# Optimization experiments

Hardware: AMD Instinct MI355X
Metric: run time of the kernel (lower is better)

The kernel has to match this reference:

```python
import jax, jax.numpy as jnp
import numpy as np
import math

B, S, D = 4, 1024, 1024
H, DH = 16, 64
DFF = 4 * D
NEG = -1e9


def _layernorm(x, g, b, eps=1e-5):
    mu = jnp.mean(x, axis=-1, keepdims=True)
    var = jnp.var(x, axis=-1, keepdims=True)
    return (x - mu) * jax.lax.rsqrt(var + eps) * g + b


def setup_inputs() -> dict:
    key = jax.random.key(0)
    ks = jax.random.split(key, 12)
    inp = {
        "input": jax.random.normal(ks[0], (B, S, D), dtype=jnp.float32),
        # additive causal mask: 0 on/below diagonal, -1e9 above
        "causal_mask": jnp.where(
            jnp.tril(jnp.ones((S, S), dtype=bool)), 0.0, NEG
        ).astype(jnp.float32)[None, None],
        # additive padding mask: last 64 tokens of each sequence are padding
        "padding_mask": jnp.where(jnp.arange(S) < S - 64, 0.0, NEG)
        .astype(jnp.float32)[None, None, None, :]
        .repeat(B, axis=0),
        "ln1_g": jnp.ones((D,), jnp.float32), "ln1_b": jnp.zeros((D,), jnp.float32),
        "ln2_g": jnp.ones((D,), jnp.float32), "ln2_b": jnp.zeros((D,), jnp.float32),
        "ln3_g": jnp.ones((D,), jnp.float32), "ln3_b": jnp.zeros((D,), jnp.float32),
        "Wq": jax.random.normal(ks[1], (D, H * DH), jnp.float32) * 0.02,
        "bq": jnp.zeros((H * DH,), jnp.float32),
        "Wk": jax.random.normal(ks[2], (D, H * DH), jnp.float32) * 0.02,
        "bk": jnp.zeros((H * DH,), jnp.float32),
        "Wv": jax.random.normal(ks[3], (D, H * DH), jnp.float32) * 0.02,
        "bv": jnp.zeros((H * DH,), jnp.float32),
        "Wo": jax.random.normal(ks[4], (H * DH, D), jnp.float32) * 0.02,
        "bo": jnp.zeros((D,), jnp.float32),
        "W1": jax.random.normal(ks[5], (D, DFF), jnp.float32) * 0.02,
        "b1": jnp.zeros((DFF,), jnp.float32),
        "W2": jax.random.normal(ks[6], (DFF, D), jnp.float32) * 0.02,
        "b2": jnp.zeros((D,), jnp.float32),
    }
    return inp


def reference(input, causal_mask, padding_mask,
              ln1_g, ln1_b, ln2_g, ln2_b, ln3_g, ln3_b,
              Wq, bq, Wk, bk, Wv, bv, Wo, bo, W1, b1, W2, b2):
    x = _layernorm(input, ln1_g, ln1_b)
    b, s, _ = x.shape

    def heads(y):  # [b,s,H*DH] -> [b,H,s,DH]
        return y.reshape(b, s, H, DH).transpose(0, 2, 1, 3)

    q = heads(x @ Wq + bq)
    k = heads(x @ Wk + bk)
    v = heads(x @ Wv + bv)

    logits = jnp.einsum('bhqd,bhkd->bhqk', q, k) / math.sqrt(DH)
    logits = logits + causal_mask + padding_mask
    probs = jax.nn.softmax(logits, axis=-1)
    attn = jnp.einsum('bhqk,bhkd->bhqd', probs, v)
    attn = attn.transpose(0, 2, 1, 3).reshape(b, s, H * DH)  # b s (h d)
    attn_out = attn @ Wo + bo

    x = x + _layernorm(attn_out, ln2_g, ln2_b)
    h = _layernorm(x, ln3_g, ln3_b)
    x = x + (jax.nn.gelu(h @ W1 + b1, approximate=False) @ W2 + b2)
    return x
```

## Files before the change

kernel.cpp:

```cpp
#include <hip/hip_runtime.h>
#include <hip/hip_bf16.h>

typedef __hip_bfloat16 bf16;
typedef __bf16 bf16x8 __attribute__((ext_vector_type(8)));
typedef float f32x4 __attribute__((ext_vector_type(4)));

#define DEV __device__ __forceinline__

DEV int swz(int r, int k) { return r * 64 + (k ^ ((r & 7) << 3)); }

#define GLOAD_LDS16(gaddr, laddr)                                              \
  __builtin_amdgcn_global_load_lds(                                            \
      (const __attribute__((address_space(1))) void*)(gaddr),                  \
      (__attribute__((address_space(3))) void*)(laddr), 16, 0, 0)

__global__ void prep_kernel(
    const float* __restrict__ Wq, const float* __restrict__ Wk,
    const float* __restrict__ Wv, const float* __restrict__ Wo,
    const float* __restrict__ bq, const float* __restrict__ bk,
    const float* __restrict__ bv,
    bf16* __restrict__ WqkvT, bf16* __restrict__ WoT, float* __restrict__ bqkv,
    const float* __restrict__ in, const float* __restrict__ g1,
    const float* __restrict__ b1v, float* __restrict__ xo, bf16* __restrict__ xb) {
  __shared__ bf16 t[32][33];
  __shared__ float ss[4], qq[4];
  int bid = blockIdx.x;
  if (bid >= 4108) {
    int row = bid - 4108, tid = threadIdx.y * 32 + threadIdx.x;
    int lane = tid & 63, w = tid >> 6;
    float4 v = reinterpret_cast<const float4*>(in + (size_t)row * 1024)[tid];
    float s = v.x + v.y + v.z + v.w;
    float sq = v.x * v.x + v.y * v.y + v.z * v.z + v.w * v.w;
#pragma unroll
    for (int m = 32; m; m >>= 1) { s += __shfl_xor(s, m); sq += __shfl_xor(sq, m); }
    if (lane == 0) { ss[w] = s; qq[w] = sq; }
    __syncthreads();
    s = ss[0] + ss[1] + ss[2] + ss[3];
    sq = qq[0] + qq[1] + qq[2] + qq[3];
    float mu = s * (1.f / 1024.f);
    float rs = rsqrtf(sq * (1.f / 1024.f) - mu * mu + 1e-5f);
    float4 gg = reinterpret_cast<const float4*>(g1)[tid];
    float4 bb = reinterpret_cast<const float4*>(b1v)[tid];
    float4 y;
    y.x = (v.x - mu) * rs * gg.x + bb.x;
    y.y = (v.y - mu) * rs * gg.y + bb.y;
    y.z = (v.z - mu) * rs * gg.z + bb.z;
    y.w = (v.w - mu) * rs * gg.w + bb.w;
    reinterpret_cast<float4*>(xo + (size_t)row * 1024)[tid] = y;
    union { bf16 h[4]; uint2 u; } pk;
    pk.h[0] = __float2bfloat16(y.x); pk.h[1] = __float2bfloat16(y.y);
    pk.h[2] = __float2bfloat16(y.z); pk.h[3] = __float2bfloat16(y.w);
    reinterpret_cast<uint2*>(xb + (size_t)row * 1024)[tid] = pk.u;
    return;
  }
  if (bid >= 4096) {
    int i = (bid - 4096) * 256 + threadIdx.y * 32 + threadIdx.x;
    if (i < 3072)
      bqkv[i] = i < 1024 ? bq[i] : (i < 2048 ? bk[i - 1024] : bv[i - 2048]);
    return;
  }
  int wsel = bid >> 10;
  const float* src = wsel == 0 ? Wq : wsel == 1 ? Wk : wsel == 2 ? Wv : Wo;
  bf16* dst = wsel < 3 ? WqkvT + (size_t)wsel * 1048576 : WoT;
  int tb = bid & 1023;
  int bx = (tb & 31) * 32, by = (tb >> 5) * 32;
  int tx = threadIdx.x, ty = threadIdx.y;
#pragma unroll
  for (int j = 0; j < 32; j += 8)
    t[ty + j][tx] = __float2bfloat16(src[(size_t)(by + ty + j) * 1024 + bx + tx]);
  __syncthreads();
#pragma unroll
  for (int j = 0; j < 32; j += 8)
    dst[(size_t)(bx + ty + j) * 1024 + by + tx] = t[tx][ty + j];
}

__global__ __launch_bounds__(256) void ln23_kernel(
    const float* __restrict__ x, const float* __restrict__ ao,
    const float* __restrict__ g2, const float* __restrict__ b2,
    const float* __restrict__ g3, const float* __restrict__ b3,
    float* __restrict__ x2o, bf16* __restrict__ hb) {
  int row = blockIdx.x, tid = threadIdx.x;
  int lane = tid & 63, w = tid >> 6;
  float4 a = reinterpret_cast<const float4*>(ao + (size_t)row * 1024)[tid];
  float s = a.x + a.y + a.z + a.w;
  float sq = a.x * a.x + a.y * a.y + a.z * a.z + a.w * a.w;
#pragma unroll
  for (int m = 32; m; m >>= 1) { s += __shfl_xor(s, m); sq += __shfl_xor(sq, m); }
  __shared__ float s1[4], q1[4], s2[4], q2[4];
  if (lane == 0) { s1[w] = s; q1[w] = sq; }
  __syncthreads();
  s = s1[0] + s1[1] + s1[2] + s1[3];
  sq = q1[0] + q1[1] + q1[2] + q1[3];
  float mu = s * (1.f / 1024.f);
  float rs = rsqrtf(sq * (1.f / 1024.f) - mu * mu + 1e-5f);
  float4 xr = reinterpret_cast<const float4*>(x + (size_t)row * 1024)[tid];
  float4 gg = reinterpret_cast<const float4*>(g2)[tid];
  float4 bb = reinterpret_cast<const float4*>(b2)[tid];
  float4 x2;
  x2.x = xr.x + (a.x - mu) * rs * gg.x + bb.x;
  x2.y = xr.y + (a.y - mu) * rs * gg.y + bb.y;
  x2.z = xr.z + (a.z - mu) * rs * gg.z + bb.z;
  x2.w = xr.w + (a.w - mu) * rs * gg.w + bb.w;
  reinterpret_cast<float4*>(x2o + (size_t)row * 1024)[tid] = x2;
  s = x2.x + x2.y + x2.z + x2.w;
  sq = x2.x * x2.x + x2.y * x2.y + x2.z * x2.z + x2.w * x2.w;
#pragma unroll
  for (int m = 32; m; m >>= 1) { s += __shfl_xor(s, m); sq += __shfl_xor(sq, m); }
  if (lane == 0) { s2[w] = s; q2[w] = sq; }
  __syncthreads();
  s = s2[0] + s2[1] + s2[2] + s2[3];
  sq = q2[0] + q2[1] + q2[2] + q2[3];
  mu = s * (1.f / 1024.f);
  rs = rsqrtf(sq * (1.f / 1024.f) - mu * mu + 1e-5f);
  gg = reinterpret_cast<const float4*>(g3)[tid];
  bb = reinterpret_cast<const float4*>(b3)[tid];
  union { bf16 h[4]; uint2 u; } pk;
  pk.h[0] = __float2bfloat16((x2.x - mu) * rs * gg.x + bb.x);
  pk.h[1] = __float2bfloat16((x2.y - mu) * rs * gg.y + bb.y);
  pk.h[2] = __float2bfloat16((x2.z - mu) * rs * gg.z + bb.z);
  pk.h[3] = __float2bfloat16((x2.w - mu) * rs * gg.w + bb.w);
  reinterpret_cast<uint2*>(hb + (size_t)row * 1024)[tid] = pk.u;
}

template <int BM, int BN, int WM, int WN, int MINW,
          bool GELU, bool RES, bool OUTBF, bool VSPLIT>
__global__ __launch_bounds__(WM * WN * 64, MINW) void gemm_db(
    const bf16* __restrict__ A, const bf16* __restrict__ BT,
    const float* __restrict__ bias, const float* __restrict__ res,
    float* __restrict__ outf, bf16* __restrict__ outb,
    bf16* __restrict__ kt, bf16* __restrict__ vt,
    int M, int N, int K) {
  constexpr int NW = WM * WN;
  constexpr int MT = BM / WM / 16, NT = BN / WN / 16;
  constexpr int ACH = BM / 8, BCH = BN / 8;
  constexpr int PW = (ACH + BCH) / NW;
  __shared__ __align__(16) bf16 As[2][BM * 64];
  __shared__ __align__(16) bf16 Bs[2][BN * 64];
  const int t = threadIdx.x, lane = t & 63, w = t >> 6;
  const int wr = w / WN, wc = w % WN;
  const int l15 = lane & 15, l4 = lane >> 4;
  const int gx = gridDim.x, nwg = gx * gridDim.y;
  int bid = blockIdx.y * gx + blockIdx.x;
  int sbid = (bid & 7) * (nwg >> 3) + (bid >> 3);
  const int m0 = (sbid / gx) * BM, n0 = (sbid % gx) * BN;
  const int lr = lane >> 3;
  const int scol = ((lane & 7) * 8) ^ (lr * 8);

  auto stage = [&](int buf, int kt_) {
    const int k0 = kt_ << 6;
#pragma unroll
    for (int i = 0; i < PW; ++i) {
      int c = w * PW + i;
      if (c < ACH) {
        GLOAD_LDS16(A + (size_t)(m0 + c * 8 + lr) * K + k0 + scol, &As[buf][c * 512]);
      } else {
        int c2 = c - ACH;
        GLOAD_LDS16(BT + (size_t)(n0 + c2 * 8 + lr) * K + k0 + scol, &Bs[buf][c2 * 512]);
      }
    }
  };

  f32x4 acc[MT][NT] = {};
  const int nk = K >> 6;
  stage(0, 0);
  __syncthreads();
  int cur = 0;
  for (int kk = 0; kk < nk; ++kk) {
    if (kk + 1 < nk) stage(cur ^ 1, kk + 1);
#pragma unroll
    for (int ks = 0; ks < 2; ++ks) {
      bf16x8 af[MT], bfr[NT];
#pragma unroll
      for (int m = 0; m < MT; ++m)
        af[m] = *reinterpret_cast<const bf16x8*>(
            &As[cur][swz(wr * (BM / WM) + m * 16 + l15, ks * 32 + l4 * 8)]);
#pragma unroll
      for (int n = 0; n < NT; ++n)
        bfr[n] = *reinterpret_cast<const bf16x8*>(
            &Bs[cur][swz(wc * (BN / WN) + n * 16 + l15, ks * 32 + l4 * 8)]);
      __builtin_amdgcn_s_setprio(1);
#pragma unroll
      for (int m = 0; m < MT; ++m)
#pragma unroll
        for (int n = 0; n < NT; ++n)
          acc[m][n] = __builtin_amdgcn_mfma_f32_16x16x32_bf16(af[m], bfr[n], acc[m][n], 0, 0, 0);
      __builtin_amdgcn_s_setprio(0);
    }
    __syncthreads();
    cur ^= 1;
  }

#pragma unroll
  for (int m = 0; m < MT; ++m) {
    int gr0 = m0 + wr * (BM / WM) + m * 16 + l4 * 4;
#pragma unroll
    for (int n = 0; n < NT; ++n) {
      int gc = n0 + wc * (BN / WN) + n * 16 + l15;
      float bv = bias[gc];
#pragma unroll
      for (int q = 0; q < 4; ++q) {
        int gr = gr0 + q;
        float v = acc[m][n][q] + bv;
        if constexpr (GELU) v = 0.5f * v * (1.f + erff(v * 0.70710678118654752f));
        if constexpr (RES) v += res[(size_t)gr * N + gc];
        if constexpr (VSPLIT) {
          int s = gr & 1023, bb = gr >> 10;
          if (gc < 1024) {
            outb[(size_t)gr * N + gc] = __float2bfloat16(v);
          } else if (gc < 2048) {
            int hd = gc - 1024, hh = hd >> 6, d = hd & 63;
            int ln = (s & 15) | (((d >> 3) & 3) << 4);
            kt[(((size_t)(bb * 16 + hh) * 64 + (s >> 4)) << 10) + (d >> 5) * 512 +
               ln * 8 + (d & 7)] = __float2bfloat16(v);
          } else {
            int hd = gc - 2048, hh = hd >> 6, d = hd & 63;
            int ln = (d & 15) | (((s >> 3) & 3) << 4);
            vt[(((size_t)(bb * 16 + hh) * 4 + (d >> 4)) << 14) + ((s >> 5) << 9) +
               ln * 8 + (s & 7)] = __float2bfloat16(v);
          }
        } else if constexpr (OUTBF) {
          outb[(size_t)gr * N + gc] = __float2bfloat16(v);
        } else {
          outf[(size_t)gr * N + gc] = v;
        }
      }
    }
  }
}

__global__ __launch_bounds__(256, 2) void attn_kernel(
    const bf16* __restrict__ qkv, const bf16* __restrict__ kt,
    const bf16* __restrict__ vt, bf16* __restrict__ o,
    const float* __restrict__ W1, const float* __restrict__ W2,
    bf16* __restrict__ W1T, bf16* __restrict__ W2T) {
  const int S = 1024, QS = 3072, HD = 1024;
  constexpr int PSTR = 72;
  __shared__ __align__(16) bf16 P[4][16 * PSTR];
  __shared__ bf16 tt[32][33];
  int bid = blockIdx.x;
  const int t = threadIdx.x, lane = t & 63, w = t >> 6;
  if (bid >= 512) {
    int b2 = bid - 512;
    const float* src; bf16* dst; int K, N, tb;
    if (b2 < 4096) { src = W1; dst = W1T; K = 1024; N = 4096; tb = b2; }
    else           { src = W2; dst = W2T; K = 4096; N = 1024; tb = b2 - 4096; }
    int ntx = N >> 5;
    int bx = (tb % ntx) * 32, by = (tb / ntx) * 32;
    int tx = t & 31, ty = t >> 5;
#pragma unroll
    for (int j = 0; j < 32; j += 8)
      tt[ty + j][tx] = __float2bfloat16(src[(size_t)(by + ty + j) * N + bx + tx]);
    __syncthreads();
#pragma unroll
    for (int j = 0; j < 32; j += 8)
      dst[(size_t)(bx + ty + j) * K + by + tx] = tt[tx][ty + j];
    return;
  }
  int xcd = bid & 7, j = bid >> 3;
  int grp = xcd * 8 + (j >> 3);
  int pr = j & 7;
  const int b = grp >> 4, h = grp & 15;
  const int l15 = lane & 15, l4 = lane >> 4;

  const bf16* qg = qkv;
  const int bh = b * 16 + h;
  const bf16* kbase = kt + ((size_t)bh << 16) + lane * 8;
  const bf16* vbase = vt + ((size_t)bh << 16) + lane * 8;

  bf16x8 kA[8], kB[8];
  auto loadK = [&](int kb, bf16x8* kf) {
#pragma unroll
    for (int cb = 0; cb < 4; ++cb)
#pragma unroll
      for (int ks = 0; ks < 2; ++ks)
        kf[cb * 2 + ks] = *reinterpret_cast<const bf16x8*>(
            kbase + (((kb >> 4) + cb) << 10) + (ks << 9));
  };

  auto run_strip = [&](int q0) {
    bf16x8 qf0, qf1;
    {
      const bf16* qp = qg + (size_t)(b * S + q0 + l15) * QS + h * 64 + l4 * 8;
      qf0 = *reinterpret_cast<const bf16x8*>(qp);
      qf1 = *reinterpret_cast<const bf16x8*>(qp + 32);
    }
    f32x4 acc[4] = {};
    float mrow = -1e30f, lrow = 0.f;
    const int kmaxa = q0 + 15, kmax = kmaxa < 959 ? kmaxa : 959;
    const int nt = (kmax >> 6) + 1;
    loadK(0, kA);

    for (int kt_ = 0; kt_ < nt; ++kt_) {
      const int kb = kt_ << 6;
      bf16x8* kf = (kt_ & 1) ? kB : kA;
      bf16x8* kn = (kt_ & 1) ? kA : kB;
      bf16x8 vf[8];
#pragma unroll
      for (int n = 0; n < 4; ++n)
#pragma unroll
        for (int ks = 0; ks < 2; ++ks)
          vf[n * 2 + ks] = *reinterpret_cast<const bf16x8*>(
              vbase + (n << 14) + (((kb >> 5) + ks) << 9));
      if (kt_ + 1 < nt) loadK(kb + 64, kn);

      f32x4 sc[4];
      __builtin_amdgcn_s_setprio(1);
#pragma unroll
      for (int cb = 0; cb < 4; ++cb) {
        f32x4 z = {};
        z = __builtin_amdgcn_mfma_f32_16x16x32_bf16(kf[cb * 2 + 0], qf0, z, 0, 0, 0);
        z = __builtin_amdgcn_mfma_f32_16x16x32_bf16(kf[cb * 2 + 1], qf1, z, 0, 0, 0);
        sc[cb] = z;
      }
      __builtin_amdgcn_s_setprio(0);

      const int q = q0 + l15;
      float p[16];
#pragma unroll
      for (int cb = 0; cb < 4; ++cb)
#pragma unroll
        for (int r = 0; r < 4; ++r) {
          int kgl = kb + cb * 16 + l4 * 4 + r;
          p[cb * 4 + r] = (kgl > q) ? -1e30f : sc[cb][r] * 0.125f;
        }
      float tm = p[0];
#pragma unroll
      for (int i = 1; i < 16; ++i) tm = fmaxf(tm, p[i]);
      tm = fmaxf(tm, __shfl_xor(tm, 16));
      tm = fmaxf(tm, __shfl_xor(tm, 32));
      bool defer = __all(tm <= mrow + 8.f);
      float mn = defer ? mrow : fmaxf(mrow, tm);
      float ps = 0.f;
#pragma unroll
      for (int i = 0; i < 16; ++i) { p[i] = __expf(p[i] - mn); ps += p[i]; }
      ps += __shfl_xor(ps, 16);
      ps += __shfl_xor(ps, 32);
      if (defer) {
        lrow += ps;
      } else {
        float al = __expf(mrow - mn);
        mrow = mn;
        lrow = lrow * al + ps;
#pragma unroll
        for (int n = 0; n < 4; ++n)
#pragma unroll
          for (int r = 0; r < 4; ++r) acc[n][r] *= al;
      }
#pragma unroll
      for (int cb = 0; cb < 4; ++cb) {
        union { bf16 h4[4]; uint2 u; } pk;
#pragma unroll
        for (int r = 0; r < 4; ++r) pk.h4[r] = __float2bfloat16(p[cb * 4 + r]);
        *reinterpret_cast<uint2*>(&P[w][l15 * PSTR + cb * 16 + l4 * 4]) = pk.u;
      }
      asm volatile("" ::: "memory");
      bf16x8 pb0 = *reinterpret_cast<const bf16x8*>(&P[w][l15 * PSTR + l4 * 8]);
      bf16x8 pb1 = *reinterpret_cast<const bf16x8*>(&P[w][l15 * PSTR + 32 + l4 * 8]);
      __builtin_amdgcn_s_setprio(1);
#pragma unroll
      for (int n = 0; n < 4; ++n) {
        acc[n] = __builtin_amdgcn_mfma_f32_16x16x32_bf16(vf[n * 2 + 0], pb0, acc[n], 0, 0, 0);
        acc[n] = __builtin_amdgcn_mfma_f32_16x16x32_bf16(vf[n * 2 + 1], pb1, acc[n], 0, 0, 0);
      }
      __builtin_amdgcn_s_setprio(0);
    }

    float inv = 1.f / lrow;
#pragma unroll
    for (int n = 0; n < 4; ++n) {
      union { bf16 h4[4]; uint2 u; } pk;
#pragma unroll
      for (int r = 0; r < 4; ++r) pk.h4[r] = __float2bfloat16(acc[n][r] * inv);
      *reinterpret_cast<uint2*>(&P[w][l15 * PSTR + n * 16 + l4 * 4]) = pk.u;
    }
    asm volatile("" ::: "memory");
    {
      int qq = lane >> 2, c = lane & 3;
#pragma unroll
      for (int i = 0; i < 2; ++i) {
        uint4 ov = *reinterpret_cast<const uint4*>(&P[w][qq * PSTR + c * 16 + i * 8]);
        *reinterpret_cast<uint4*>(
            o + (size_t)(b * S + q0 + qq) * HD + h * 64 + c * 16 + i * 8) = ov;
      }
    }
    asm volatile("" ::: "memory");
  };

  run_strip(pr * 64 + w * 16);
  run_strip((15 - pr) * 64 + w * 16);
}

extern "C" void kernel_launch(void* const* d_in, const int* in_sizes, int n_in,
                              void* d_out, int out_size, void* d_ws, size_t ws_size,
                              hipStream_t stream) {
  const float* input = (const float*)d_in[0];
  const float* ln1g = (const float*)d_in[3];
  const float* ln1b = (const float*)d_in[4];
  const float* ln2g = (const float*)d_in[5];
  const float* ln2b = (const float*)d_in[6];
  const float* ln3g = (const float*)d_in[7];
  const float* ln3b = (const float*)d_in[8];
  const float* Wq = (const float*)d_in[9];  const float* bq = (const float*)d_in[10];
  const float* Wk = (const float*)d_in[11]; const float* bk = (const float*)d_in[12];
  const float* Wv = (const float*)d_in[13]; const float* bv = (const float*)d_in[14];
  const float* Wo = (const float*)d_in[15]; const float* bo = (const float*)d_in[16];
  const float* W1 = (const float*)d_in[17]; const float* b1 = (const float*)d_in[18];
  const float* W2 = (const float*)d_in[19]; const float* b2 = (const float*)d_in[20];

  const int M = 4096, D = 1024, F = 4096;
  char* p = (char*)d_ws;
  size_t off = 0;
  auto nxt = [&](size_t n) { char* r = p + off; off += n; return r; };
  bf16* WqkvT = (bf16*)nxt((size_t)3 * D * D * 2);
  bf16* WoT = (bf16*)nxt((size_t)D * D * 2);
  bf16* W1T = (bf16*)nxt((size_t)F * D * 2);
  bf16* W2T = (bf16*)nxt((size_t)D * F * 2);
  float* bqkv = (float*)nxt(16384);
  float* xf  = (float*)nxt((size_t)M * D * 4);
  float* aof = (float*)nxt((size_t)M * D * 4);
  float* x2f = (float*)nxt((size_t)M * D * 4);
  bf16* xb = (bf16*)nxt((size_t)M * D * 2);
  bf16* qkv = (bf16*)nxt((size_t)M * 3 * D * 2);
  bf16* ktb = (bf16*)aof;
  bf16* vtb = (bf16*)((char*)aof + (size_t)8 * 1024 * 1024);
  bf16* gb = (bf16*)xf;
  bf16* ab = xb;
  bf16* hb = qkv;

  prep_kernel<<<4108 + 4096, dim3(32, 8), 0, stream>>>(
      Wq, Wk, Wv, Wo, bq, bk, bv, WqkvT, WoT, bqkv,
      input, ln1g, ln1b, xf, xb);

  gemm_db<256, 192, 2, 4, 1, false, false, true, true>
      <<<dim3(16, 16), 512, 0, stream>>>(
      xb, WqkvT, bqkv, nullptr, nullptr, qkv, ktb, vtb, M, 3 * D, D);

  attn_kernel<<<512 + 8192, 256, 0, stream>>>(qkv, ktb, vtb, ab, W1, W2, W1T, W2T);

  gemm_db<128, 64, 2, 2, 4, false, false, false, false>
      <<<dim3(16, 32), 256, 0, stream>>>(
      ab, WoT, bo, nullptr, aof, nullptr, nullptr, nullptr, M, D, D);

  ln23_kernel<<<M, 256, 0, stream>>>(xf, aof, ln2g, ln2b, ln3g, ln3b, x2f, hb);

  gemm_db<256, 256, 2, 4, 2, true, false, true, false>
      <<<dim3(16, 16), 512, 0, stream>>>(
      hb, W1T, b1, nullptr, nullptr, gb, nullptr, nullptr, M, F, D);
  gemm_db<128, 64, 2, 2, 4, false, true, false, false>
      <<<dim3(16, 32), 256, 0, stream>>>(
      gb, W2T, b2, x2f, (float*)d_out, nullptr, nullptr, nullptr, M, D, F);
}
```

Before: 214.7 us.

## Move W1/W2 transpose blocks from attention kernel into QKV GEMM launch

The fp32-to-bf16 transposes of W1 and W2 used to run as 8192 extra blocks appended to the attention kernel. They now run as 4096 extra blocks in z-slices of the QKV GEMM grid, each 512-thread block handling two 32x32 tiles. This lets the attention kernel run alone and overlaps the weight conversion with the QKV GEMM. In exchange the GEMM grid becomes much larger, and its LDS allocation may limit how many transpose blocks can co-reside.

```diff
diff --git a/kernel.cpp b/kernel.cpp
--- a/kernel.cpp
+++ b/kernel.cpp
@@ -123,20 +123,45 @@
 }
 
 template <int BM, int BN, int WM, int WN, int MINW,
-          bool GELU, bool RES, bool OUTBF, bool VSPLIT>
+          bool GELU, bool RES, bool OUTBF, bool VSPLIT, bool TP>
 __global__ __launch_bounds__(WM * WN * 64, MINW) void gemm_db(
     const bf16* __restrict__ A, const bf16* __restrict__ BT,
     const float* __restrict__ bias, const float* __restrict__ res,
     float* __restrict__ outf, bf16* __restrict__ outb,
     bf16* __restrict__ kt, bf16* __restrict__ vt,
+    const float* __restrict__ TW1, const float* __restrict__ TW2,
+    bf16* __restrict__ TW1T, bf16* __restrict__ TW2T,
     int M, int N, int K) {
   constexpr int NW = WM * WN;
   constexpr int MT = BM / WM / 16, NT = BN / WN / 16;
   constexpr int ACH = BM / 8, BCH = BN / 8;
   constexpr int PW = (ACH + BCH) / NW;
+  const int t = threadIdx.x;
+  if constexpr (TP) {
+    if (blockIdx.z > 0) {
+      __shared__ bf16 tt[2][32][33];
+      int zi = blockIdx.z - 1;
+      int g = t >> 8;
+      int tile = (zi * 256 + blockIdx.y * 16 + blockIdx.x) * 2 + g;
+      const float* src; bf16* dst; int K2, N2, tb;
+      if (tile < 4096) { src = TW1; dst = TW1T; K2 = 1024; N2 = 4096; tb = tile; }
+      else             { src = TW2; dst = TW2T; K2 = 4096; N2 = 1024; tb = tile - 4096; }
+      int ntx = N2 >> 5;
+      int bx = (tb % ntx) * 32, by = (tb / ntx) * 32;
+      int tx = t & 31, ty = (t >> 5) & 7;
+#pragma unroll
+      for (int j = 0; j < 32; j += 8)
+        tt[g][ty + j][tx] = __float2bfloat16(src[(size_t)(by + ty + j) * N2 + bx + tx]);
+      __syncthreads();
+#pragma unroll
+      for (int j = 0; j < 32; j += 8)
+        dst[(size_t)(bx + ty + j) * K2 + by + tx] = tt[g][tx][ty + j];
+      return;
+    }
+  }
   __shared__ __align__(16) bf16 As[2][BM * 64];
   __shared__ __align__(16) bf16 Bs[2][BN * 64];
-  const int t = threadIdx.x, lane = t & 63, w = t >> 6;
+  const int lane = t & 63, w = t >> 6;
   const int wr = w / WN, wc = w % WN;
   const int l15 = lane & 15, l4 = lane >> 4;
   const int gx = gridDim.x, nwg = gx * gridDim.y;
@@ -230,39 +255,20 @@
 
 __global__ __launch_bounds__(256, 2) void attn_kernel(
     const bf16* __restrict__ qkv, const bf16* __restrict__ kt,
-    const bf16* __restrict__ vt, bf16* __restrict__ o,
-    const float* __restrict__ W1, const float* __restrict__ W2,
-    bf16* __restrict__ W1T, bf16* __restrict__ W2T) {
+    const bf16* __restrict__ vt, bf16* __restrict__ o) {
   const int S = 1024, QS = 3072, HD = 1024;
-  constexpr int PSTR = 72;
-  __shared__ __align__(16) bf16 P[4][16 * PSTR];
-  __shared__ bf16 tt[32][33];
+  const bf16* qg = qkv;
   int bid = blockIdx.x;
-  const int t = threadIdx.x, lane = t & 63, w = t >> 6;
-  if (bid >= 512) {
-    int b2 = bid - 512;
-    const float* src; bf16* dst; int K, N, tb;
-    if (b2 < 4096) { src = W1; dst = W1T; K = 1024; N = 4096; tb = b2; }
-    else           { src = W2; dst = W2T; K = 4096; N = 1024; tb = b2 - 4096; }
-    int ntx = N >> 5;
-    int bx = (tb % ntx) * 32, by = (tb / ntx) * 32;
-    int tx = t & 31, ty = t >> 5;
-#pragma unroll
-    for (int j = 0; j < 32; j += 8)
-      tt[ty + j][tx] = __float2bfloat16(src[(size_t)(by + ty + j) * N + bx + tx]);
-    __syncthreads();
-#pragma unroll
-    for (int j = 0; j < 32; j += 8)
-      dst[(size_t)(bx + ty + j) * K + by + tx] = tt[tx][ty + j];
-    return;
-  }
   int xcd = bid & 7, j = bid >> 3;
   int grp = xcd * 8 + (j >> 3);
   int pr = j & 7;
   const int b = grp >> 4, h = grp & 15;
+  const int t = threadIdx.x, lane = t & 63, w = t >> 6;
   const int l15 = lane & 15, l4 = lane >> 4;
 
-  const bf16* qg = qkv;
+  constexpr int PSTR = 72;
+  __shared__ __align__(16) bf16 P[4][16 * PSTR];
+
   const int bh = b * 16 + h;
   const bf16* kbase = kt + ((size_t)bh << 16) + lane * 8;
   const bf16* vbase = vt + ((size_t)bh << 16) + lane * 8;
@@ -431,22 +437,26 @@
       Wq, Wk, Wv, Wo, bq, bk, bv, WqkvT, WoT, bqkv,
       input, ln1g, ln1b, xf, xb);
 
-  gemm_db<256, 192, 2, 4, 1, false, false, true, true>
+  gemm_db<256, 192, 2, 4, 1, false, false, true, true, true>
+      <<<dim3(16, 16, 17), 512, 0, stream>>>(
+      xb, WqkvT, bqkv, nullptr, nullptr, qkv, ktb, vtb,
+      W1, W2, W1T, W2T, M, 3 * D, D);
+
+  attn_kernel<<<512, 256, 0, stream>>>(qkv, ktb, vtb, ab);
+
+  gemm_db<128, 64, 2, 2, 4, false, false, false, false, false>
+      <<<dim3(16, 32), 256, 0, stream>>>(
+      ab, WoT, bo, nullptr, aof, nullptr, nullptr, nullptr,
+      nullptr, nullptr, nullptr, nullptr, M, D, D);
+
+  ln23_kernel<<<M, 256, 0, stream>>>(xf, aof, ln2g, ln2b, ln3g, ln3b, x2f, hb);
+
+  gemm_db<256, 256, 2, 4, 2, true, false, true, false, false>
       <<<dim3(16, 16), 512, 0, stream>>>(
-      xb, WqkvT, bqkv, nullptr, nullptr, qkv, ktb, vtb, M, 3 * D, D);
-
-  attn_kernel<<<512 + 8192, 256, 0, stream>>>(qkv, ktb, vtb, ab, W1, W2, W1T, W2T);
-
-  gemm_db<128, 64, 2, 2, 4, false, false, false, false>
+      hb, W1T, b1, nullptr, nullptr, gb, nullptr, nullptr,
+      nullptr, nullptr, nullptr, nullptr, M, F, D);
+  gemm_db<128, 64, 2, 2, 4, false, true, false, false, false>
       <<<dim3(16, 32), 256, 0, stream>>>(
-      ab, WoT, bo, nullptr, aof, nullptr, nullptr, nullptr, M, D, D);
-
-  ln23_kernel<<<M, 256, 0, stream>>>(xf, aof, ln2g, ln2b, ln3g, ln3b, x2f, hb);
-
-  gemm_db<256, 256, 2, 4, 2, true, false, true, false>
-      <<<dim3(16, 16), 512, 0, stream>>>(
-      hb, W1T, b1, nullptr, nullptr, gb, nullptr, nullptr, M, F, D);
-  gemm_db<128, 64, 2, 2, 4, false, true, false, false>
-      <<<dim3(16, 32), 256, 0, stream>>>(
-      gb, W2T, b2, x2f, (float*)d_out, nullptr, nullptr, nullptr, M, D, F);
+      gb, W2T, b2, x2f, (float*)d_out, nullptr, nullptr, nullptr,
+      nullptr, nullptr, nullptr, nullptr, M, D, F);
 }
```

Result: no change. 217.5 us (+1.3%).
